# Kernel optimization log

Measured on AMD Instinct MI355X. Metric: run time of the kernel, lower is better.

The kernel has to match this reference:

```python
import jax, jax.numpy as jnp
import numpy as np

N_VARS = 16
BATCH = 16
SEQ = 512
P = N_VARS * (N_VARS - 1)  # ordered pairs i != j


def setup_inputs() -> dict:
    key = jax.random.key(0)
    ks = jax.random.split(key, 12)
    n = N_VARS

    def w(k, shape, fan_in):
        return jax.random.normal(k, shape, dtype=jnp.float32) / np.sqrt(fan_in)

    z = lambda *s: jnp.zeros(s, jnp.float32)
    return {
        'data': jax.random.normal(ks[0], (BATCH, SEQ, n), dtype=jnp.float32),
        # structure learner: n*n -> 256 -> 128 -> n*n (dropout skipped / eval mode)
        'Ws1': w(ks[1], (n * n, 256), n * n), 'bs1': z(256),
        'Ws2': w(ks[2], (256, 128), 256), 'bs2': z(128),
        'Ws3': w(ks[3], (128, n * n), 128), 'bs3': z(n * n),
        # per-variable causal mechanisms (stacked): (n-1) -> 128 -> 64 -> 1
        'Wm1': w(ks[4], (n, n - 1, 128), n - 1), 'bm1': z(n, 128),
        'Wm2': w(ks[5], (n, 128, 64), 128), 'bm2': z(n, 64),
        'Wm3': w(ks[6], (n, 64), 64), 'bm3': z(n),
        # per-pair independence tests (stacked): 2 -> 32 -> 1, sigmoid
        'Wt1': w(ks[7], (P, 2, 32), 2), 'bt1': z(P, 32),
        'Wt2': w(ks[8], (P, 32), 32), 'bt2': z(P),
    }


def reference(data, Ws1, bs1, Ws2, bs2, Ws3, bs3,
              Wm1, bm1, Wm2, bm2, Wm3, bm3,
              Wt1, bt1, Wt2, bt2):
    B, S, n = data.shape
    N = B * S
    flat = data.reshape(N, n)  # [N, n] all samples

    # ---- correlations of batch-averaged series (vectorized corrcoef) ----
    avg = data.mean(axis=0)                    # [S, n]
    xc = avg - avg.mean(axis=0, keepdims=True)
    cov = xc.T @ xc                            # [n, n]
    std = jnp.sqrt(jnp.clip(jnp.diag(cov), 0.0))
    denom = std[:, None] * std[None, :]
    corr = jnp.abs(jnp.where(denom > 0, cov / jnp.where(denom > 0, denom, 1.0), 0.0))
    corr = corr * (1.0 - jnp.eye(n, dtype=corr.dtype))  # zero diagonal (i != j only)

    # ---- structure learner MLP -> sigmoid -> strict upper-tri DAG mask ----
    h = jax.nn.relu(corr.reshape(1, -1) @ Ws1 + bs1)
    h = jax.nn.relu(h @ Ws2 + bs2)
    adj = jax.nn.sigmoid(h @ Ws3 + bs3).reshape(n, n)
    adj = jnp.triu(adj, 1)

    # ---- causal mechanisms: gather-parents -> per-var MLP -> scatter ----
    idx = np.stack([[j for j in range(n) if j != v] for v in range(n)])  # [n, n-1]
    pmask = adj > 0.5
    parent_mask = pmask[idx, np.arange(n)[:, None]].astype(flat.dtype)   # [n, n-1]
    inp = flat[:, idx] * parent_mask[None]                               # [N, n, n-1]
    h1 = jax.nn.relu(jnp.einsum('nvp,vph->nvh', inp, Wm1) + bm1)         # [N, n, 128]
    h2 = jax.nn.relu(jnp.einsum('nvh,vhk->nvk', h1, Wm2) + bm2)          # [N, n, 64]
    mech = jnp.einsum('nvk,vk->nv', h2, Wm3) + bm3                       # [N, n]
    has_parents = parent_mask.sum(axis=1) > 0                            # [n]
    predictions = jnp.where(has_parents[None, :], mech, flat).reshape(B, S, n)

    # ---- batched per-pair independence tests ----
    pairs = np.array([(i, j) for i in range(n) for j in range(n) if i != j])
    pi, pj = pairs[:, 0], pairs[:, 1]
    X = jnp.stack([flat[:, pi], flat[:, pj]], axis=-1)                   # [N, P, 2]
    ht = jax.nn.relu(jnp.einsum('npc,pch->nph', X, Wt1) + bt1)           # [N, P, 32]
    s = jax.nn.sigmoid(jnp.einsum('nph,ph->np', ht, Wt2) + bt2).mean(axis=0)  # [P]
    scores = jnp.zeros((n, n), flat.dtype).at[pi, pj].set(s)

    return adj, predictions, scores
```

## Files before the change

kernel.cpp:

```cpp
#include <hip/hip_runtime.h>
#include <hip/hip_bf16.h>


typedef __attribute__((ext_vector_type(8))) short bf16x8;
typedef __attribute__((ext_vector_type(4))) short bf16x4;
typedef __attribute__((ext_vector_type(4))) float f32x4;

#define DEV __device__ __forceinline__
DEV short f2bf(float f){ __hip_bfloat16 h = __float2bfloat16(f); short s; __builtin_memcpy(&s,&h,2); return s; }

struct GraphSm {
    float avT[16 * 532];
    float part[512];
    float corr[256];
    float h1[256];
    float h2[128];
    float adj[256];
};
struct MechSm {
    short W2T[64 * 136];
    short H1[8][16 * 136];
    float W1[16 * 128];
    float B1[128];
    float B2[64];
    float W3[64];
};
struct PairSm {
    float w0[2][32], w1[2][32], bb[2][32], w2[2][32];
    float red[2][512];
    float b2s[2];
};
union SmU { GraphSm g; MechSm m; PairSm p; };

__global__ void __launch_bounds__(512, 2) k_fused(
    const float* __restrict__ data,
    const float* __restrict__ Ws1, const float* __restrict__ bs1,
    const float* __restrict__ Ws2, const float* __restrict__ bs2,
    const float* __restrict__ Ws3, const float* __restrict__ bs3,
    const float* __restrict__ Wm1, const float* __restrict__ bm1,
    const float* __restrict__ Wm2, const float* __restrict__ bm2,
    const float* __restrict__ Wm3, const float* __restrict__ bm3,
    const float* __restrict__ Wt1, const float* __restrict__ bt1,
    const float* __restrict__ Wt2, const float* __restrict__ bt2,
    float* __restrict__ out)
{
    __shared__ __align__(16) SmU sm;
    int tid = threadIdx.x, bid = blockIdx.x;

    if (bid >= 128) {
        int pb = bid - 128;
        int p0 = pb*2, p1 = p0 + 1;
        int i0 = p0 / 15, jr0 = p0 % 15;
        int j0 = jr0 + (jr0 >= i0 ? 1 : 0);
        int i1 = p1 / 15, jr1 = p1 % 15;
        int j1 = jr1 + (jr1 >= i1 ? 1 : 0);
        if (tid < 64) {
            int pp = tid >> 5, h = tid & 31;
            int p = pb*2 + pp;
            sm.p.w0[pp][h] = Wt1[p*64 + h];
            sm.p.w1[pp][h] = Wt1[p*64 + 32 + h];
            sm.p.bb[pp][h] = bt1[p*32 + h];
            sm.p.w2[pp][h] = Wt2[p*32 + h];
        }
        if (tid < 2) sm.p.b2s[tid] = bt2[pb*2 + tid];
        __syncthreads();
        float b2s0 = sm.p.b2s[0], b2s1 = sm.p.b2s[1];
        float acc0 = 0.f, acc1 = 0.f;
        float nxa0, nxb0, nxa1, nxb1;
        {
            int s = ((bid & 15) * 512) + tid;
            nxa0 = data[s*16 + i0]; nxb0 = data[s*16 + j0];
            nxa1 = data[s*16 + i1]; nxb1 = data[s*16 + j1];
        }
        for (int it = 0; it < 16; ++it) {
            float xa0 = nxa0, xb0 = nxb0, xa1 = nxa1, xb1 = nxb1;
            if (it < 15) {
                int s = (((it + 1 + bid) & 15) * 512) + tid;
                nxa0 = data[s*16 + i0]; nxb0 = data[s*16 + j0];
                nxa1 = data[s*16 + i1]; nxb1 = data[s*16 + j1];
            }
            float za0=0.f, zb0=0.f, za1=0.f, zb1=0.f;
            #pragma unroll
            for (int h = 0; h < 32; h += 2) {
                float t00 = fmaf(xa0, sm.p.w0[0][h],   fmaf(xb0, sm.p.w1[0][h],   sm.p.bb[0][h]));
                za0 = fmaf(fmaxf(t00, 0.f), sm.p.w2[0][h],   za0);
                float t01 = fmaf(xa0, sm.p.w0[0][h+1], fmaf(xb0, sm.p.w1[0][h+1], sm.p.bb[0][h+1]));
                zb0 = fmaf(fmaxf(t01, 0.f), sm.p.w2[0][h+1], zb0);
                float t10 = fmaf(xa1, sm.p.w0[1][h],   fmaf(xb1, sm.p.w1[1][h],   sm.p.bb[1][h]));
                za1 = fmaf(fmaxf(t10, 0.f), sm.p.w2[1][h],   za1);
                float t11 = fmaf(xa1, sm.p.w0[1][h+1], fmaf(xb1, sm.p.w1[1][h+1], sm.p.bb[1][h+1]));
                zb1 = fmaf(fmaxf(t11, 0.f), sm.p.w2[1][h+1], zb1);
            }
            float z0 = b2s0 + za0 + zb0;
            float z1 = b2s1 + za1 + zb1;
            acc0 += __builtin_amdgcn_rcpf(1.f + __expf(-z0));
            acc1 += __builtin_amdgcn_rcpf(1.f + __expf(-z1));
        }
        sm.p.red[0][tid] = acc0;
        sm.p.red[1][tid] = acc1;
        __syncthreads();
        for (int off = 256; off > 0; off >>= 1) {
            if (tid < off) {
                sm.p.red[0][tid] += sm.p.red[0][tid + off];
                sm.p.red[1][tid] += sm.p.red[1][tid + off];
            }
            __syncthreads();
        }
        if (tid == 0) {
            out[256 + 131072 + i0*16 + j0] = sm.p.red[0][0] * (1.f/8192.f);
            out[256 + 131072 + i1*16 + j1] = sm.p.red[1][0] * (1.f/8192.f);
        }
        return;
    }

    int v = bid >> 3, chunk = bid & 7;
    int gs0 = chunk * 1024;

    float pf_wm1[4];
    {
        #pragma unroll
        for (int r = 0; r < 4; ++r) {
            int e = tid + 512*r;
            int k = e >> 7, h = e & 127;
            pf_wm1[r] = 0.f;
            if (k != v) {
                int p = k - (k > v ? 1 : 0);
                pf_wm1[r] = Wm1[v*1920 + p*128 + h];
            }
        }
    }
    float4 pf_wm2[4];
    {
        const float* wp = Wm2 + v*8192 + tid*16;
        #pragma unroll
        for (int m4 = 0; m4 < 4; ++m4) pf_wm2[m4] = *(const float4*)&wp[m4*4];
    }
    float b1r  = bm1[v*128 + (tid & 127)];
    float b2r_ = bm2[v*64  + (tid & 63)];
    float w3r  = Wm3[v*64  + (tid & 63)];
    float bm3v = bm3[v];
    float bs1r = bs1[tid & 255];
    float bs2r = bs2[tid & 127];
    float bs3r = bs3[tid & 255];

    {
        int vb = (tid & 3) * 4;
        int sgr = ((tid >> 2) + bid*4) & 127;
        for (int k = 0; k < 4; ++k) {
            int s = sgr + k*128;
            float ax=0.f, ay=0.f, az=0.f, aw=0.f;
            #pragma unroll
            for (int b = 0; b < 16; ++b) {
                float4 d4 = *(const float4*)&data[b*8192 + s*16 + vb];
                ax += d4.x; ay += d4.y; az += d4.z; aw += d4.w;
            }
            sm.g.avT[(vb+0)*532 + s] = ax * 0.0625f;
            sm.g.avT[(vb+1)*532 + s] = ay * 0.0625f;
            sm.g.avT[(vb+2)*532 + s] = az * 0.0625f;
            sm.g.avT[(vb+3)*532 + s] = aw * 0.0625f;
        }
    }
    __syncthreads();
    if (tid < 128) {
        int vv = tid >> 3, sgm = tid & 7;
        const float* rp = &sm.g.avT[vv*532 + sgm*64];
        float a0=0.f, a1=0.f, a2=0.f, a3=0.f;
        for (int s = 0; s < 64; s += 4) {
            float4 fa = *(const float4*)&rp[s];
            a0 += fa.x; a1 += fa.y; a2 += fa.z; a3 += fa.w;
        }
        sm.g.h2[tid] = (a0+a1)+(a2+a3);
    }
    __syncthreads();
    int ci, cj; float mci, mcj;
    {
        int t = tid & 255, hh = tid >> 8;
        ci = t >> 4; cj = t & 15;
        mci = 0.f; mcj = 0.f;
        #pragma unroll
        for (int q = 0; q < 8; ++q) { mci += sm.g.h2[ci*8 + q]; mcj += sm.g.h2[cj*8 + q]; }
        mci *= (1.f/512.f); mcj *= (1.f/512.f);
        const float* pi_ = &sm.g.avT[ci*532 + hh*256];
        const float* pj_ = &sm.g.avT[cj*532 + hh*256];
        float a0=0.f, a1=0.f, a2=0.f, a3=0.f;
        #pragma unroll 8
        for (int s = 0; s < 256; s += 4) {
            float4 fa = *(const float4*)&pi_[s];
            float4 fb = *(const float4*)&pj_[s];
            a0 = fmaf(fa.x, fb.x, a0); a1 = fmaf(fa.y, fb.y, a1);
            a2 = fmaf(fa.z, fb.z, a2); a3 = fmaf(fa.w, fb.w, a3);
        }
        sm.g.part[tid] = (a0+a1)+(a2+a3);
    }
    __syncthreads();
    if (tid < 256) {
        float cij = sm.g.part[tid] + sm.g.part[256 + tid] - 512.f*mci*mcj;
        float cii = sm.g.part[ci*17] + sm.g.part[256 + ci*17] - 512.f*mci*mci;
        float cjj = sm.g.part[cj*17] + sm.g.part[256 + cj*17] - 512.f*mcj*mcj;
        float den = sqrtf(fmaxf(cii, 0.f)) * sqrtf(fmaxf(cjj, 0.f));
        sm.g.corr[tid] = (den > 0.f && ci != cj) ? fabsf(cij/den) : 0.f;
    }
    __syncthreads();

    float* red2 = sm.g.avT;

    {
        int o4 = tid & 63, ks = tid >> 6;
        int o4e = (o4 + bid*4) & 63;
        const float* W1p = Ws1 + ks*32*256 + o4e*4;
        const float* cp  = sm.g.corr + ks*32;
        float ax=0.f, ay=0.f, az=0.f, aw=0.f;
        float bx=0.f, by=0.f, bz=0.f, bw=0.f;
        #pragma unroll 8
        for (int i = 0; i < 32; i += 2) {
            float4 w0 = *(const float4*)&W1p[(i  )*256];
            float4 w1 = *(const float4*)&W1p[(i+1)*256];
            float c0 = cp[i], c1 = cp[i+1];
            ax=fmaf(c0,w0.x,ax); ay=fmaf(c0,w0.y,ay); az=fmaf(c0,w0.z,az); aw=fmaf(c0,w0.w,aw);
            bx=fmaf(c1,w1.x,bx); by=fmaf(c1,w1.y,by); bz=fmaf(c1,w1.z,bz); bw=fmaf(c1,w1.w,bw);
        }
        float4 r4; r4.x=ax+bx; r4.y=ay+by; r4.z=az+bz; r4.w=aw+bw;
        *(float4*)&red2[ks*256 + o4e*4] = r4;
    }
    __syncthreads();
    if (tid < 256) {
        float s = bs1r;
        #pragma unroll
        for (int k2 = 0; k2 < 8; ++k2) s += red2[k2*256 + tid];
        sm.g.h1[tid] = fmaxf(s, 0.f);
    }
    __syncthreads();
    {
        int o4 = tid & 31, ks = tid >> 5;
        int o4e = (o4 + bid*2) & 31;
        const float* W2p = Ws2 + ks*16*128 + o4e*4;
        const float* cp  = sm.g.h1 + ks*16;
        float ax=0.f, ay=0.f, az=0.f, aw=0.f;
        float bx=0.f, by=0.f, bz=0.f, bw=0.f;
        #pragma unroll
        for (int i = 0; i < 16; i += 2) {
            float4 w0 = *(const float4*)&W2p[(i  )*128];
            float4 w1 = *(const float4*)&W2p[(i+1)*128];
            float c0 = cp[i], c1 = cp[i+1];
            ax=fmaf(c0,w0.x,ax); ay=fmaf(c0,w0.y,ay); az=fmaf(c0,w0.z,az); aw=fmaf(c0,w0.w,aw);
            bx=fmaf(c1,w1.x,bx); by=fmaf(c1,w1.y,by); bz=fmaf(c1,w1.z,bz); bw=fmaf(c1,w1.w,bw);
        }
        float4 r4; r4.x=ax+bx; r4.y=ay+by; r4.z=az+bz; r4.w=aw+bw;
        *(float4*)&red2[ks*128 + o4e*4] = r4;
    }
    __syncthreads();
    if (tid < 128) {
        float s = bs2r;
        #pragma unroll
        for (int k2 = 0; k2 < 16; ++k2) s += red2[k2*128 + tid];
        sm.g.h2[tid] = fmaxf(s, 0.f);
    }
    __syncthreads();
    {
        int o4 = tid & 63, ks = tid >> 6;
        int o4e = (o4 + bid*4) & 63;
        const float* W3p = Ws3 + ks*16*256 + o4e*4;
        const float* cp  = sm.g.h2 + ks*16;
        float ax=0.f, ay=0.f, az=0.f, aw=0.f;
        float bx=0.f, by=0.f, bz=0.f, bw=0.f;
        #pragma unroll
        for (int i = 0; i < 16; i += 2) {
            float4 w0 = *(const float4*)&W3p[(i  )*256];
            float4 w1 = *(const float4*)&W3p[(i+1)*256];
            float c0 = cp[i], c1 = cp[i+1];
            ax=fmaf(c0,w0.x,ax); ay=fmaf(c0,w0.y,ay); az=fmaf(c0,w0.z,az); aw=fmaf(c0,w0.w,aw);
            bx=fmaf(c1,w1.x,bx); by=fmaf(c1,w1.y,by); bz=fmaf(c1,w1.z,bz); bw=fmaf(c1,w1.w,bw);
        }
        float4 r4; r4.x=ax+bx; r4.y=ay+by; r4.z=az+bz; r4.w=aw+bw;
        *(float4*)&red2[ks*256 + o4e*4] = r4;
    }
    __syncthreads();
    if (tid < 256) {
        float z = bs3r;
        #pragma unroll
        for (int k2 = 0; k2 < 8; ++k2) z += red2[k2*256 + tid];
        float a = 1.f / (1.f + expf(-z));
        int r = tid >> 4, cc = tid & 15;
        float adjv = (r < cc) ? a : 0.f;
        sm.g.adj[tid] = adjv;
        if (bid == 0) out[tid] = adjv;
    }
    if (bid == 0 && tid >= 256 && tid < 272)
        out[256 + 131072 + (tid-256)*17] = 0.f;
    __syncthreads();

    #pragma unroll
    for (int r = 0; r < 4; ++r) {
        int e = tid + 512*r;
        int k = e >> 7;
        float val = 0.f;
        if (k != v && sm.g.adj[k*16 + v] > 0.5f) val = pf_wm1[r];
        sm.m.W1[e] = val;
    }
    float hp = 0.f;
    #pragma unroll
    for (int k = 0; k < 16; ++k)
        if (k != v && sm.g.adj[k*16 + v] > 0.5f) hp = 1.f;
    #pragma unroll
    for (int m4 = 0; m4 < 4; ++m4) {
        float4 w4 = pf_wm2[m4];
        int e0 = tid*16 + m4*4;
        int h = e0 >> 6;
        int jj0 = e0 & 63;
        sm.m.W2T[(jj0+0)*136 + h] = f2bf(w4.x);
        sm.m.W2T[(jj0+1)*136 + h] = f2bf(w4.y);
        sm.m.W2T[(jj0+2)*136 + h] = f2bf(w4.z);
        sm.m.W2T[(jj0+3)*136 + h] = f2bf(w4.w);
    }
    if (tid < 128) sm.m.B1[tid] = b1r;
    else if (tid < 192) sm.m.B2[tid - 128] = b2r_;
    else if (tid < 256) sm.m.W3[tid - 192] = w3r;
    __syncthreads();

    int lane = tid & 63, wid = tid >> 6;
    int c = lane & 15, q = lane >> 4;

    bf16x8 a1f[8];
    #pragma unroll
    for (int ht = 0; ht < 8; ++ht) {
        #pragma unroll
        for (int jj = 0; jj < 8; ++jj) {
            int k = q*8 + jj;
            float w = (k < 16) ? sm.m.W1[k*128 + ht*16 + c] : 0.f;
            a1f[ht][jj] = f2bf(w);
        }
    }
    bf16x8 b2r[16];
    #pragma unroll
    for (int jt = 0; jt < 4; ++jt)
        #pragma unroll
        for (int ks = 0; ks < 4; ++ks)
            b2r[jt*4 + ks] = *(const bf16x8*)&sm.m.W2T[(jt*16 + c)*136 + ks*32 + q*8];
    float w3c[4], b2c[4];
    #pragma unroll
    for (int jt = 0; jt < 4; ++jt) { w3c[jt] = sm.m.W3[jt*16 + c]; b2c[jt] = sm.m.B2[jt*16 + c]; }

    short* h1buf = sm.m.H1[wid];
    bool act = (q < 2);

    float4 u0c, u1c;
    {
        int st0 = wid*8;
        if (act) {
            const float* xp = &data[(gs0 + st0*16 + c)*16 + q*8];
            u0c = *(const float4*)xp;
            u1c = *(const float4*)(xp + 4);
        }
    }

    for (int stl = 0; stl < 8; ++stl) {
        int st = wid*8 + stl;
        float4 u0 = u0c, u1 = u1c;
        if (stl < 7 && act) {
            const float* xp = &data[(gs0 + (st+1)*16 + c)*16 + q*8];
            u0c = *(const float4*)xp;
            u1c = *(const float4*)(xp + 4);
        }
        bf16x8 xb;
        #pragma unroll
        for (int i2 = 0; i2 < 8; ++i2) xb[i2] = 0;
        if (act) {
            xb[0] = f2bf(u0.x); xb[1] = f2bf(u0.y);
            xb[2] = f2bf(u0.z); xb[3] = f2bf(u0.w);
            xb[4] = f2bf(u1.x); xb[5] = f2bf(u1.y);
            xb[6] = f2bf(u1.z); xb[7] = f2bf(u1.w);
        }
        f32x4 c1[8];
        #pragma unroll
        for (int ht = 0; ht < 8; ++ht) c1[ht] = *(const f32x4*)&sm.m.B1[ht*16 + q*4];
        #pragma unroll
        for (int ht = 0; ht < 8; ++ht)
            c1[ht] = __builtin_amdgcn_mfma_f32_16x16x32_bf16(a1f[ht], xb, c1[ht], 0, 0, 0);
        #pragma unroll
        for (int ht = 0; ht < 8; ++ht) {
            bf16x4 pk;
            #pragma unroll
            for (int r = 0; r < 4; ++r) pk[r] = f2bf(fmaxf(c1[ht][r], 0.f));
            *(bf16x4*)&h1buf[c*136 + ht*16 + q*4] = pk;
        }
        f32x4 c2[4];
        #pragma unroll
        for (int jt = 0; jt < 4; ++jt) {
            float bi = b2c[jt];
            c2[jt] = (f32x4){bi, bi, bi, bi};
        }
        #pragma unroll
        for (int ks = 0; ks < 4; ++ks) {
            bf16x8 a2 = *(const bf16x8*)&h1buf[c*136 + ks*32 + q*8];
            #pragma unroll
            for (int jt = 0; jt < 4; ++jt)
                c2[jt] = __builtin_amdgcn_mfma_f32_16x16x32_bf16(a2, b2r[jt*4 + ks], c2[jt], 0, 0, 0);
        }
        float part[4];
        #pragma unroll
        for (int r = 0; r < 4; ++r) part[r] = 0.f;
        #pragma unroll
        for (int jt = 0; jt < 4; ++jt)
            #pragma unroll
            for (int r = 0; r < 4; ++r)
                part[r] = fmaf(fmaxf(c2[jt][r], 0.f), w3c[jt], part[r]);
        #pragma unroll
        for (int off = 1; off < 16; off <<= 1)
            #pragma unroll
            for (int r = 0; r < 4; ++r)
                part[r] += __shfl_xor(part[r], off, 16);
        if (c == 0) {
            #pragma unroll
            for (int r = 0; r < 4; ++r) {
                int s_loc = st*16 + q*4 + r;
                float mech = part[r] + bm3v;
                float xv = data[(gs0 + s_loc)*16 + v];
                out[256 + (gs0 + s_loc)*16 + v] = (hp != 0.f) ? mech : xv;
            }
        }
    }
}

extern "C" void kernel_launch(void* const* d_in, const int* in_sizes, int n_in,
                              void* d_out, int out_size, void* d_ws, size_t ws_size,
                              hipStream_t stream)
{
    const float* data = (const float*)d_in[0];
    const float* Ws1  = (const float*)d_in[1];
    const float* bs1  = (const float*)d_in[2];
    const float* Ws2  = (const float*)d_in[3];
    const float* bs2  = (const float*)d_in[4];
    const float* Ws3  = (const float*)d_in[5];
    const float* bs3  = (const float*)d_in[6];
    const float* Wm1  = (const float*)d_in[7];
    const float* bm1  = (const float*)d_in[8];
    const float* Wm2  = (const float*)d_in[9];
    const float* bm2  = (const float*)d_in[10];
    const float* Wm3  = (const float*)d_in[11];
    const float* bm3  = (const float*)d_in[12];
    const float* Wt1  = (const float*)d_in[13];
    const float* bt1  = (const float*)d_in[14];
    const float* Wt2  = (const float*)d_in[15];
    const float* bt2  = (const float*)d_in[16];
    float* out = (float*)d_out;
    (void)d_ws; (void)ws_size; (void)in_sizes; (void)n_in; (void)out_size;

    hipLaunchKernelGGL(k_fused, dim3(248), dim3(512), 0, stream,
                       data, Ws1, bs1, Ws2, bs2, Ws3, bs3,
                       Wm1, bm1, Wm2, bm2, Wm3, bm3,
                       Wt1, bt1, Wt2, bt2, out);
}
```

Baseline: 126.3 us.

## Prefetch structure-MLP weights into registers, shuffle reductions, deeper pair prefetch

Ws2 and Ws3 slices are loaded into registers before the correlation and first-layer phases, so those global loads overlap earlier work. The pair-test blocks get a two-iteration-deep data prefetch, and their shared-memory tree reduction becomes a wave shuffle reduction with a single barrier. Launch bounds drop from 2 to 1 blocks per SM to make room for the extra registers, and the per-block staggering of access offsets is removed. This cuts barriers and load latency but may lower occupancy and bring back contention on the same cache lines across blocks.

After: 138.6 us. 1.1x slower.

```diff
diff --git a/kernel.cpp b/kernel.cpp
--- a/kernel.cpp
+++ b/kernel.cpp
@@ -27,12 +27,12 @@
 };
 struct PairSm {
     float w0[2][32], w1[2][32], bb[2][32], w2[2][32];
-    float red[2][512];
+    float red0[8], red1[8];
     float b2s[2];
 };
 union SmU { GraphSm g; MechSm m; PairSm p; };
 
-__global__ void __launch_bounds__(512, 2) k_fused(
+__global__ void __launch_bounds__(512, 1) k_fused(
     const float* __restrict__ data,
     const float* __restrict__ Ws1, const float* __restrict__ bs1,
     const float* __restrict__ Ws2, const float* __restrict__ bs2,
@@ -49,10 +49,10 @@
 
     if (bid >= 128) {
         int pb = bid - 128;
-        int p0 = pb*2, p1 = p0 + 1;
+        int p0 = pb*2, p1p = p0 + 1;
         int i0 = p0 / 15, jr0 = p0 % 15;
         int j0 = jr0 + (jr0 >= i0 ? 1 : 0);
-        int i1 = p1 / 15, jr1 = p1 % 15;
+        int i1 = p1p / 15, jr1 = p1p % 15;
         int j1 = jr1 + (jr1 >= i1 ? 1 : 0);
         if (tid < 64) {
             int pp = tid >> 5, h = tid & 31;
@@ -66,18 +66,22 @@
         __syncthreads();
         float b2s0 = sm.p.b2s[0], b2s1 = sm.p.b2s[1];
         float acc0 = 0.f, acc1 = 0.f;
-        float nxa0, nxb0, nxa1, nxb1;
+        float a0A, b0A, a1A, b1A, a0B, b0B, a1B, b1B;
         {
-            int s = ((bid & 15) * 512) + tid;
-            nxa0 = data[s*16 + i0]; nxb0 = data[s*16 + j0];
-            nxa1 = data[s*16 + i1]; nxb1 = data[s*16 + j1];
+            int s0 = tid;
+            a0A = data[s0*16 + i0]; b0A = data[s0*16 + j0];
+            a1A = data[s0*16 + i1]; b1A = data[s0*16 + j1];
+            int s1 = 512 + tid;
+            a0B = data[s1*16 + i0]; b0B = data[s1*16 + j0];
+            a1B = data[s1*16 + i1]; b1B = data[s1*16 + j1];
         }
         for (int it = 0; it < 16; ++it) {
-            float xa0 = nxa0, xb0 = nxb0, xa1 = nxa1, xb1 = nxb1;
-            if (it < 15) {
-                int s = (((it + 1 + bid) & 15) * 512) + tid;
-                nxa0 = data[s*16 + i0]; nxb0 = data[s*16 + j0];
-                nxa1 = data[s*16 + i1]; nxb1 = data[s*16 + j1];
+            float xa0 = a0A, xb0 = b0A, xa1 = a1A, xb1 = b1A;
+            a0A = a0B; b0A = b0B; a1A = a1B; b1A = b1B;
+            if (it < 14) {
+                int s = (it + 2)*512 + tid;
+                a0B = data[s*16 + i0]; b0B = data[s*16 + j0];
+                a1B = data[s*16 + i1]; b1B = data[s*16 + j1];
             }
             float za0=0.f, zb0=0.f, za1=0.f, zb1=0.f;
             #pragma unroll
@@ -96,19 +100,20 @@
             acc0 += __builtin_amdgcn_rcpf(1.f + __expf(-z0));
             acc1 += __builtin_amdgcn_rcpf(1.f + __expf(-z1));
         }
-        sm.p.red[0][tid] = acc0;
-        sm.p.red[1][tid] = acc1;
+        #pragma unroll
+        for (int off = 32; off > 0; off >>= 1) {
+            acc0 += __shfl_xor(acc0, off);
+            acc1 += __shfl_xor(acc1, off);
+        }
+        int lane = tid & 63, wid = tid >> 6;
+        if (lane == 0) { sm.p.red0[wid] = acc0; sm.p.red1[wid] = acc1; }
         __syncthreads();
-        for (int off = 256; off > 0; off >>= 1) {
-            if (tid < off) {
-                sm.p.red[0][tid] += sm.p.red[0][tid + off];
-                sm.p.red[1][tid] += sm.p.red[1][tid + off];
-            }
-            __syncthreads();
-        }
         if (tid == 0) {
-            out[256 + 131072 + i0*16 + j0] = sm.p.red[0][0] * (1.f/8192.f);
-            out[256 + 131072 + i1*16 + j1] = sm.p.red[1][0] * (1.f/8192.f);
+            float s0 = 0.f, s1 = 0.f;
+            #pragma unroll
+            for (int w = 0; w < 8; ++w) { s0 += sm.p.red0[w]; s1 += sm.p.red1[w]; }
+            out[256 + 131072 + i0*16 + j0] = s0 * (1.f/8192.f);
+            out[256 + 131072 + i1*16 + j1] = s1 * (1.f/8192.f);
         }
         return;
     }
@@ -117,16 +122,14 @@
     int gs0 = chunk * 1024;
 
     float pf_wm1[4];
-    {
-        #pragma unroll
-        for (int r = 0; r < 4; ++r) {
-            int e = tid + 512*r;
-            int k = e >> 7, h = e & 127;
-            pf_wm1[r] = 0.f;
-            if (k != v) {
-                int p = k - (k > v ? 1 : 0);
-                pf_wm1[r] = Wm1[v*1920 + p*128 + h];
-            }
+    #pragma unroll
+    for (int r = 0; r < 4; ++r) {
+        int e = tid + 512*r;
+        int k = e >> 7, h = e & 127;
+        pf_wm1[r] = 0.f;
+        if (k != v) {
+            int p = k - (k > v ? 1 : 0);
+            pf_wm1[r] = Wm1[v*1920 + p*128 + h];
         }
     }
     float4 pf_wm2[4];
@@ -144,10 +147,9 @@
     float bs3r = bs3[tid & 255];
 
     {
-        int vb = (tid & 3) * 4;
-        int sgr = ((tid >> 2) + bid*4) & 127;
+        int vb = (tid & 3) * 4, sg = tid >> 2;
         for (int k = 0; k < 4; ++k) {
-            int s = sgr + k*128;
+            int s = sg + k*128;
             float ax=0.f, ay=0.f, az=0.f, aw=0.f;
             #pragma unroll
             for (int b = 0; b < 16; ++b) {
@@ -161,6 +163,22 @@
         }
     }
     __syncthreads();
+
+    float4 pw2[16];
+    {
+        int o4 = tid & 31, ks = tid >> 5;
+        const float* W2p = Ws2 + ks*16*128 + o4*4;
+        #pragma unroll
+        for (int i = 0; i < 16; ++i) pw2[i] = *(const float4*)&W2p[i*128];
+    }
+    float4 pw3[16];
+    {
+        int o4 = tid & 63, ks = tid >> 6;
+        const float* W3p = Ws3 + ks*16*256 + o4*4;
+        #pragma unroll
+        for (int i = 0; i < 16; ++i) pw3[i] = *(const float4*)&W3p[i*256];
+    }
+
     if (tid < 128) {
         int vv = tid >> 3, sgm = tid & 7;
         const float* rp = &sm.g.avT[vv*532 + sgm*64];
@@ -183,7 +201,7 @@
         const float* pi_ = &sm.g.avT[ci*532 + hh*256];
         const float* pj_ = &sm.g.avT[cj*532 + hh*256];
         float a0=0.f, a1=0.f, a2=0.f, a3=0.f;
-        #pragma unroll 8
+        #pragma unroll 4
         for (int s = 0; s < 256; s += 4) {
             float4 fa = *(const float4*)&pi_[s];
             float4 fb = *(const float4*)&pj_[s];
@@ -206,12 +224,11 @@
 
     {
         int o4 = tid & 63, ks = tid >> 6;
-        int o4e = (o4 + bid*4) & 63;
-        const float* W1p = Ws1 + ks*32*256 + o4e*4;
+        const float* W1p = Ws1 + ks*32*256 + o4*4;
         const float* cp  = sm.g.corr + ks*32;
         float ax=0.f, ay=0.f, az=0.f, aw=0.f;
         float bx=0.f, by=0.f, bz=0.f, bw=0.f;
-        #pragma unroll 8
+        #pragma unroll 4
         for (int i = 0; i < 32; i += 2) {
             float4 w0 = *(const float4*)&W1p[(i  )*256];
             float4 w1 = *(const float4*)&W1p[(i+1)*256];
@@ -220,7 +237,7 @@
             bx=fmaf(c1,w1.x,bx); by=fmaf(c1,w1.y,by); bz=fmaf(c1,w1.z,bz); bw=fmaf(c1,w1.w,bw);
         }
         float4 r4; r4.x=ax+bx; r4.y=ay+by; r4.z=az+bz; r4.w=aw+bw;
-        *(float4*)&red2[ks*256 + o4e*4] = r4;
+        *(float4*)&red2[ks*256 + o4*4] = r4;
     }
     __syncthreads();
     if (tid < 256) {
@@ -232,21 +249,19 @@
     __syncthreads();
     {
         int o4 = tid & 31, ks = tid >> 5;
-        int o4e = (o4 + bid*2) & 31;
-        const float* W2p = Ws2 + ks*16*128 + o4e*4;
         const float* cp  = sm.g.h1 + ks*16;
         float ax=0.f, ay=0.f, az=0.f, aw=0.f;
         float bx=0.f, by=0.f, bz=0.f, bw=0.f;
         #pragma unroll
         for (int i = 0; i < 16; i += 2) {
-            float4 w0 = *(const float4*)&W2p[(i  )*128];
-            float4 w1 = *(const float4*)&W2p[(i+1)*128];
+            float4 w0 = pw2[i];
+            float4 w1 = pw2[i+1];
             float c0 = cp[i], c1 = cp[i+1];
             ax=fmaf(c0,w0.x,ax); ay=fmaf(c0,w0.y,ay); az=fmaf(c0,w0.z,az); aw=fmaf(c0,w0.w,aw);
             bx=fmaf(c1,w1.x,bx); by=fmaf(c1,w1.y,by); bz=fmaf(c1,w1.z,bz); bw=fmaf(c1,w1.w,bw);
         }
         float4 r4; r4.x=ax+bx; r4.y=ay+by; r4.z=az+bz; r4.w=aw+bw;
-        *(float4*)&red2[ks*128 + o4e*4] = r4;
+        *(float4*)&red2[ks*128 + o4*4] = r4;
     }
     __syncthreads();
     if (tid < 128) {
@@ -258,21 +273,19 @@
     __syncthreads();
     {
         int o4 = tid & 63, ks = tid >> 6;
-        int o4e = (o4 + bid*4) & 63;
-        const float* W3p = Ws3 + ks*16*256 + o4e*4;
         const float* cp  = sm.g.h2 + ks*16;
         float ax=0.f, ay=0.f, az=0.f, aw=0.f;
         float bx=0.f, by=0.f, bz=0.f, bw=0.f;
         #pragma unroll
         for (int i = 0; i < 16; i += 2) {
-            float4 w0 = *(const float4*)&W3p[(i  )*256];
-            float4 w1 = *(const float4*)&W3p[(i+1)*256];
+            float4 w0 = pw3[i];
+            float4 w1 = pw3[i+1];
             float c0 = cp[i], c1 = cp[i+1];
             ax=fmaf(c0,w0.x,ax); ay=fmaf(c0,w0.y,ay); az=fmaf(c0,w0.z,az); aw=fmaf(c0,w0.w,aw);
             bx=fmaf(c1,w1.x,bx); by=fmaf(c1,w1.y,by); bz=fmaf(c1,w1.z,bz); bw=fmaf(c1,w1.w,bw);
         }
         float4 r4; r4.x=ax+bx; r4.y=ay+by; r4.z=az+bz; r4.w=aw+bw;
-        *(float4*)&red2[ks*256 + o4e*4] = r4;
+        *(float4*)&red2[ks*256 + o4*4] = r4;
     }
     __syncthreads();
     if (tid < 256) {
```
